# Kernel tuning notes

Measured on AMD Instinct MI355X. Metric: run time of the kernel, lower is better.

The kernel has to match this reference:

```python
import jax, jax.numpy as jnp
import numpy as np
import math

B, S, D = 8, 2048, 512
WINDOW = 30

def setup_inputs() -> dict:
    key = jax.random.key(0)
    ks = jax.random.split(key, 9)
    s = 1.0 / math.sqrt(D)
    return {
        "hidden_states": jax.random.normal(ks[0], (B, S, D), jnp.float32),
        "Wq": jax.random.normal(ks[1], (D, D), jnp.float32) * s,
        "bq": jax.random.normal(ks[2], (D,), jnp.float32) * s,
        "Wk": jax.random.normal(ks[3], (D, D), jnp.float32) * s,
        "bk": jax.random.normal(ks[4], (D,), jnp.float32) * s,
        "Wv": jax.random.normal(ks[5], (D, D), jnp.float32) * s,
        "bv": jax.random.normal(ks[6], (D,), jnp.float32) * s,
        "Wg": jax.random.normal(ks[7], (D, 1), jnp.float32) * s,
        "bg": jax.random.normal(ks[8], (1,), jnp.float32) * s,
    }

def reference(hidden_states, Wq, bq, Wk, bk, Wv, bv, Wg, bg):
    seq_len = hidden_states.shape[1]
    scale = math.sqrt(hidden_states.shape[-1])
    Q = hidden_states @ Wq + bq
    K = hidden_states @ Wk + bk
    V = hidden_states @ Wv + bv
    # [B, S, S] dense scores, single head
    scores = jnp.einsum('bsd,btd->bst', Q, K) / scale
    global_out = jnp.einsum('bst,btd->bsd', jax.nn.softmax(scores, axis=-1), V)
    pos = jnp.arange(seq_len)
    window_mask = jnp.abs(pos[:, None] - pos[None, :]) <= WINDOW  # [S, S]
    local_scores = scores + jnp.where(window_mask, 0.0, -1e9)
    local_out = jnp.einsum('bst,btd->bsd', jax.nn.softmax(local_scores, axis=-1), V)
    gate = jax.nn.sigmoid(hidden_states @ Wg + bg)  # [B, S, 1]
    return (1.0 - gate) * global_out + gate * local_out
```

## Files before the change

### kernel.cpp

```cpp
#include <hip/hip_runtime.h>
#include <math.h>

#define B_N   8
#define S_LEN 2048
#define D_DIM 512
#define M_TOT (B_N * S_LEN)
#define WIN   30

typedef short bf16x8 __attribute__((ext_vector_type(8)));
typedef float f32x4  __attribute__((ext_vector_type(4)));
typedef unsigned short u16;
typedef unsigned int   u32;

__device__ __forceinline__ u16 f2bf(float f) {
    union { float f; u32 u; } v; v.f = f;
    u32 r = v.u + 0x7fffu + ((v.u >> 16) & 1u);
    return (u16)(r >> 16);
}
__device__ __forceinline__ float bf2f(u16 u) {
    union { u32 u; float f; } v; v.u = ((u32)u) << 16; return v.f;
}

__device__ __forceinline__ void gl2lds(const u16* g, u16* l) {
    __builtin_amdgcn_global_load_lds((const __attribute__((address_space(1))) void*)g,
                                     (__attribute__((address_space(3))) void*)l,
                                     16, 0, 0);
}

__device__ __forceinline__ int xcd_logical() {
    const int n = gridDim.x;
    const int hb = blockIdx.x;
    return (hb & 7) * (n >> 3) + (hb >> 3);
}

#define VM_WAIT(N) asm volatile("s_waitcnt vmcnt(" #N ")" ::: "memory")
#define BAR() do { __builtin_amdgcn_s_barrier(); asm volatile("" ::: "memory"); } while (0)

__global__ __launch_bounds__(256)
void convert_gate(const float* __restrict__ X, const float* __restrict__ Wg,
                  const float* __restrict__ bg, u16* __restrict__ Xb, float* __restrict__ gate) {
    int wv = threadIdx.x >> 6, lane = threadIdx.x & 63;
    int row = blockIdx.x * 4 + wv;
    const float4* x4 = (const float4*)(X + (size_t)row * D_DIM);
    const float4* w4 = (const float4*)Wg;
    float acc = 0.f;
    ushort4 o0, o1;
    {
        float4 a = x4[lane * 2], w = w4[lane * 2];
        acc += a.x * w.x + a.y * w.y + a.z * w.z + a.w * w.w;
        o0.x = f2bf(a.x); o0.y = f2bf(a.y); o0.z = f2bf(a.z); o0.w = f2bf(a.w);
        float4 b = x4[lane * 2 + 1], v = w4[lane * 2 + 1];
        acc += b.x * v.x + b.y * v.y + b.z * v.z + b.w * v.w;
        o1.x = f2bf(b.x); o1.y = f2bf(b.y); o1.z = f2bf(b.z); o1.w = f2bf(b.w);
    }
    ushort4* xb4 = (ushort4*)(Xb + (size_t)row * D_DIM);
    xb4[lane * 2] = o0;
    xb4[lane * 2 + 1] = o1;
#pragma unroll
    for (int o = 32; o; o >>= 1) acc += __shfl_xor(acc, o);
    if (lane == 0) gate[row] = 1.f / (1.f + __expf(-(acc + bg[0])));
}

__global__ __launch_bounds__(256) void transpose_w3(const float* __restrict__ Wq, const float* __restrict__ Wk,
                                                    const float* __restrict__ Wv, u16* __restrict__ Wt3) {
    const float* W = blockIdx.z == 0 ? Wq : (blockIdx.z == 1 ? Wk : Wv);
    u16* Wt = Wt3 + (size_t)blockIdx.z * D_DIM * D_DIM;
    __shared__ float t[32][33];
    int k0 = blockIdx.x * 32, n0 = blockIdx.y * 32;
    int tx = threadIdx.x & 31, ty = threadIdx.x >> 5;
#pragma unroll
    for (int r = ty; r < 32; r += 8) t[r][tx] = W[(size_t)(k0 + r) * D_DIM + n0 + tx];
    __syncthreads();
#pragma unroll
    for (int r = ty; r < 32; r += 8) Wt[(size_t)(n0 + r) * D_DIM + k0 + tx] = f2bf(t[tx][r]);
}

__global__ __launch_bounds__(256) void pack_bias(const float* __restrict__ bq, const float* __restrict__ bk,
                                                 const float* __restrict__ bv, float* __restrict__ b3) {
    int i = blockIdx.x * 256 + threadIdx.x;
    b3[i] = bq[i]; b3[512 + i] = bk[i]; b3[1024 + i] = bv[i];
}

template<int EPI>
__global__ __launch_bounds__(512, 2)
void gemm256(const u16* __restrict__ A, const u16* __restrict__ Bt,
             int lda, int ldb, int K, int nx, int ny,
             const float* __restrict__ aux, void* __restrict__ Cv, int ldc, float scale,
             long long zA, long long zB, long long zC, long long zAux) {
    const int logical = xcd_logical();
    const int x = logical % nx;
    const int t2 = logical / nx;
    const int y = t2 % ny;
    const int z = t2 / ny;

    A   += zA * z;
    Bt  += zB * z;
    if (aux) aux += zAux * z;

    constexpr int BUF = 16384;
    __shared__ u16 smem[3 * BUF];
    const int tid  = threadIdx.x;
    const int lane = tid & 63;
    const int wave = tid >> 6;
    const int wr = wave >> 2, wc = wave & 3;
    const int m0 = y * 256, n0 = x * 256;

    f32x4 acc[8][4];
#pragma unroll
    for (int i = 0; i < 8; i++)
#pragma unroll
        for (int j = 0; j < 4; j++) acc[i][j] = (f32x4){0.f, 0.f, 0.f, 0.f};

    auto stage_h = [&](int b, int k0, int h) {
        int c2 = ((h & 1) << 9) + tid;
        int r  = c2 >> 2;
        int s  = (((c2 & 3) ^ ((c2 >> 3) & 3)) << 3);
        const u16* src = (h < 2) ? A  + (size_t)(m0 + r) * lda + (k0 + s)
                                 : Bt + (size_t)(n0 + r) * ldb + (k0 + s);
        gl2lds(src, smem + b * BUF + h * 4096 + wave * 512);
    };

    const int nt = K >> 5;
#pragma unroll
    for (int h = 0; h < 4; h++) stage_h(0, 0, h);
#pragma unroll
    for (int h = 0; h < 4; h++) stage_h(1, 32, h);

    const int ks = lane >> 4;
    for (int t = 0; t < nt; ++t) {
        const int cur = t % 3;
        const int nxt = (t + 2) % 3;
        const bool pf = (t + 2 < nt);
        const int kn = (t + 2) << 5;
        const u16* bA = smem + cur * BUF;
        const u16* bB = bA + 8192;

        bf16x8 af03[4], af47[4], b01[2], b23[2];

        if (t == nt - 1) { VM_WAIT(0); } else { VM_WAIT(4); }
        BAR();
        if (pf) stage_h(nxt, kn, 0);
#pragma unroll
        for (int n = 0; n < 2; n++) {
            int r = wc * 64 + n * 16 + (lane & 15);
            b01[n] = *(const bf16x8*)&bB[r * 32 + (ks ^ ((r >> 1) & 3)) * 8];
        }
#pragma unroll
        for (int m = 0; m < 4; m++) {
            int r = wr * 128 + m * 16 + (lane & 15);
            af03[m] = *(const bf16x8*)&bA[r * 32 + (ks ^ ((r >> 1) & 3)) * 8];
        }
        __builtin_amdgcn_s_setprio(1);
#pragma unroll
        for (int m = 0; m < 4; m++)
#pragma unroll
            for (int n = 0; n < 2; n++)
                acc[m][n] = __builtin_amdgcn_mfma_f32_16x16x32_bf16(af03[m], b01[n], acc[m][n], 0, 0, 0);
        __builtin_amdgcn_s_setprio(0);

        BAR();
        if (pf) stage_h(nxt, kn, 1);
#pragma unroll
        for (int n = 0; n < 2; n++) {
            int r = wc * 64 + (n + 2) * 16 + (lane & 15);
            b23[n] = *(const bf16x8*)&bB[r * 32 + (ks ^ ((r >> 1) & 3)) * 8];
        }
        __builtin_amdgcn_s_setprio(1);
#pragma unroll
        for (int m = 0; m < 4; m++)
#pragma unroll
            for (int n = 0; n < 2; n++)
                acc[m][n + 2] = __builtin_amdgcn_mfma_f32_16x16x32_bf16(af03[m], b23[n], acc[m][n + 2], 0, 0, 0);
        __builtin_amdgcn_s_setprio(0);

        BAR();
        if (pf) stage_h(nxt, kn, 2);
#pragma unroll
        for (int m = 0; m < 4; m++) {
            int r = wr * 128 + (m + 4) * 16 + (lane & 15);
            af47[m] = *(const bf16x8*)&bA[r * 32 + (ks ^ ((r >> 1) & 3)) * 8];
        }
        __builtin_amdgcn_s_setprio(1);
#pragma unroll
        for (int m = 0; m < 4; m++)
#pragma unroll
            for (int n = 0; n < 2; n++)
                acc[m + 4][n] = __builtin_amdgcn_mfma_f32_16x16x32_bf16(af47[m], b01[n], acc[m + 4][n], 0, 0, 0);
        __builtin_amdgcn_s_setprio(0);

        BAR();
        if (pf) stage_h(nxt, kn, 3);
        __builtin_amdgcn_s_setprio(1);
#pragma unroll
        for (int m = 0; m < 4; m++)
#pragma unroll
            for (int n = 0; n < 2; n++)
                acc[m + 4][n + 2] = __builtin_amdgcn_mfma_f32_16x16x32_bf16(af47[m], b23[n], acc[m + 4][n + 2], 0, 0, 0);
        __builtin_amdgcn_s_setprio(0);
    }

    u16* Cb = (u16*)Cv + zC * z;
#pragma unroll
    for (int m = 0; m < 8; m++) {
        int rbase = m0 + wr * 128 + m * 16 + ((lane >> 4) << 2);
#pragma unroll
        for (int n = 0; n < 4; n++) {
            int col = n0 + wc * 64 + n * 16 + (lane & 15);
#pragma unroll
            for (int rg = 0; rg < 4; rg++) {
                int row = rbase + rg;
                float v = acc[m][n][rg];
                if (EPI == 0) {
                    Cb[(size_t)row * ldc + col] = f2bf(v + aux[col]);
                } else {
                    Cb[(size_t)row * ldc + col] = f2bf(v * scale);
                }
            }
        }
    }
}

template<int EPI>
__global__ __launch_bounds__(256, 6)
void gemm_bt(const u16* __restrict__ A, const u16* __restrict__ Bt,
             int lda, int ldb, int K, int nx, int ny,
             const float* __restrict__ aux, void* __restrict__ Cv, int ldc, float scale,
             long long zA, long long zB, long long zC, long long zAux) {
    const int logical = xcd_logical();
    const int x = logical % nx;
    const int t2 = logical / nx;
    const int y = t2 % ny;
    const int z = t2 / ny;

    A   += zA * z;
    Bt  += zB * z;
    if (aux) aux += zAux * z;

    __shared__ u16 smem[3 * 8192];
    const int tid  = threadIdx.x;
    const int lane = tid & 63;
    const int wave = tid >> 6;
    const int wr = wave >> 1, wc = wave & 1;
    const int m0 = y * 128, n0 = x * 128;

    f32x4 acc[4][4];
#pragma unroll
    for (int i = 0; i < 4; i++)
#pragma unroll
        for (int j = 0; j < 4; j++) acc[i][j] = (f32x4){0.f, 0.f, 0.f, 0.f};

    const int c0 = tid, c1 = tid + 256;
    const int r0c = c0 >> 2, k0c = (((c0 & 3) ^ ((c0 >> 3) & 3)) << 3);
    const int r1c = c1 >> 2, k1c = (((c1 & 3) ^ ((c1 >> 3) & 3)) << 3);

    auto stage = [&](int b, int k0) {
        u16* dA = smem + b * 8192 + wave * 512;
        u16* dB = smem + b * 8192 + 4096 + wave * 512;
        gl2lds(A + (size_t)(m0 + r0c) * lda + (k0 + k0c), dA);
        gl2lds(A + (size_t)(m0 + r1c) * lda + (k0 + k1c), dA + 2048);
        gl2lds(Bt + (size_t)(n0 + r0c) * ldb + (k0 + k0c), dB);
        gl2lds(Bt + (size_t)(n0 + r1c) * ldb + (k0 + k1c), dB + 2048);
    };
    auto compute = [&](int b) {
        const u16* bA = smem + b * 8192;
        const u16* bB = smem + b * 8192 + 4096;
        const int ks = lane >> 4;
        bf16x8 af[4], bfr[4];
#pragma unroll
        for (int m = 0; m < 4; m++) {
            int r = wr * 64 + m * 16 + (lane & 15);
            af[m] = *(const bf16x8*)&bA[r * 32 + (ks ^ ((r >> 1) & 3)) * 8];
        }
#pragma unroll
        for (int n = 0; n < 4; n++) {
            int r = wc * 64 + n * 16 + (lane & 15);
            bfr[n] = *(const bf16x8*)&bB[r * 32 + (ks ^ ((r >> 1) & 3)) * 8];
        }
#pragma unroll
        for (int m = 0; m < 4; m++)
#pragma unroll
            for (int n = 0; n < 4; n++)
                acc[m][n] = __builtin_amdgcn_mfma_f32_16x16x32_bf16(af[m], bfr[n], acc[m][n], 0, 0, 0);
    };

    const int nt = K >> 5;
    stage(0, 0); stage(1, 32);

    int t = 0;
    for (; t < nt - 1; ++t) {
        VM_WAIT(4);
        BAR();
        if (t + 2 < nt) stage((t + 2) % 3, (t + 2) << 5);
        compute(t % 3);
    }
    VM_WAIT(0);
    BAR();
    compute((nt - 1) % 3);

    u16*   Cb = (EPI == 1) ? ((u16*)Cv + zC * z) : nullptr;
    float* Cf = (EPI == 2) ? ((float*)Cv + zC * z) : nullptr;

#pragma unroll
    for (int m = 0; m < 4; m++) {
        int rbase = m0 + wr * 64 + m * 16 + ((lane >> 4) << 2);
#pragma unroll
        for (int n = 0; n < 4; n++) {
            int col = n0 + wc * 64 + n * 16 + (lane & 15);
#pragma unroll
            for (int rg = 0; rg < 4; rg++) {
                int row = rbase + rg;
                float v = acc[m][n][rg];
                if (EPI == 1) {
                    Cb[(size_t)row * ldc + col] = f2bf(v + aux[row]);
                } else {
                    Cf[(size_t)row * ldc + col] = v * scale;
                }
            }
        }
    }
}

__global__ __launch_bounds__(256)
void softmax_fuse(u16* __restrict__ sc, const float* __restrict__ gate) {
    const int logical = xcd_logical();
    const int i = logical & (S_LEN - 1);
    const int z = logical >> 11;
    const int tid = threadIdx.x;
    const int wv = tid >> 6, lane = tid & 63;
    sc   += (size_t)z * S_LEN * S_LEN;
    gate += (size_t)z * S_LEN;

    __shared__ float r0[4], r1[4], mll[2];

    u16* scrow = sc + (size_t)i * S_LEN;
    uint4 raw = ((const uint4*)scrow)[tid];

    int jlo = i - WIN; if (jlo < 0) jlo = 0;
    int jhi = i + WIN; if (jhi > S_LEN - 1) jhi = S_LEN - 1;
    int cnt = jhi - jlo + 1;
    float bvv = (tid < cnt) ? bf2f(scrow[jlo + tid]) : -3.0e38f;
    float g = gate[i];

    float sv[8];
    sv[0] = bf2f((u16)(raw.x & 0xffff)); sv[1] = bf2f((u16)(raw.x >> 16));
    sv[2] = bf2f((u16)(raw.y & 0xffff)); sv[3] = bf2f((u16)(raw.y >> 16));
    sv[4] = bf2f((u16)(raw.z & 0xffff)); sv[5] = bf2f((u16)(raw.z >> 16));
    sv[6] = bf2f((u16)(raw.w & 0xffff)); sv[7] = bf2f((u16)(raw.w >> 16));

    float mx = fmaxf(fmaxf(fmaxf(sv[0], sv[1]), fmaxf(sv[2], sv[3])),
                     fmaxf(fmaxf(sv[4], sv[5]), fmaxf(sv[6], sv[7])));
#pragma unroll
    for (int o = 32; o; o >>= 1) mx = fmaxf(mx, __shfl_xor(mx, o));
    if (lane == 0) r0[wv] = mx;
    __syncthreads();
    float mg = fmaxf(fmaxf(r0[0], r0[1]), fmaxf(r0[2], r0[3]));

    float ev[8];
#pragma unroll
    for (int k = 0; k < 8; k++) ev[k] = __expf(sv[k] - mg);
    float se = ev[0] + ev[1] + ev[2] + ev[3] + ev[4] + ev[5] + ev[6] + ev[7];
#pragma unroll
    for (int o = 32; o; o >>= 1) se += __shfl_xor(se, o);
    if (lane == 0) r1[wv] = se;

    if (wv == 0) {
        float ml = bvv;
#pragma unroll
        for (int o = 32; o; o >>= 1) ml = fmaxf(ml, __shfl_xor(ml, o));
        float e = (lane < cnt) ? __expf(bvv - ml) : 0.f;
        float s2 = e;
#pragma unroll
        for (int o = 32; o; o >>= 1) s2 += __shfl_xor(s2, o);
        if (lane == 0) { mll[0] = ml; mll[1] = 1.f / s2; }
    }
    __syncthreads();
    float invl = (1.f - g) / (r1[0] + r1[1] + r1[2] + r1[3]);
    float ml  = mll[0];
    float ill = g * mll[1];

    const int c0 = tid * 8;
    u32 pk_[4];
#pragma unroll
    for (int h = 0; h < 4; h++) {
        float rA = ev[2 * h] * invl;
        float rB = ev[2 * h + 1] * invl;
        int colA = c0 + 2 * h;
        if ((u32)(colA - i + WIN) <= 2u * WIN)     rA += __expf(sv[2 * h] - ml) * ill;
        if ((u32)(colA + 1 - i + WIN) <= 2u * WIN) rB += __expf(sv[2 * h + 1] - ml) * ill;
        pk_[h] = (u32)f2bf(rA) | ((u32)f2bf(rB) << 16);
    }
    uint4 pw = {pk_[0], pk_[1], pk_[2], pk_[3]};
    ((uint4*)scrow)[tid] = pw;
}

extern "C" void kernel_launch(void* const* d_in, const int* in_sizes, int n_in,
                              void* d_out, int out_size, void* d_ws, size_t ws_size,
                              hipStream_t stream) {
    const float* X  = (const float*)d_in[0];
    const float* Wq = (const float*)d_in[1];
    const float* bq = (const float*)d_in[2];
    const float* Wk = (const float*)d_in[3];
    const float* bk = (const float*)d_in[4];
    const float* Wv = (const float*)d_in[5];
    const float* bv = (const float*)d_in[6];
    const float* Wg = (const float*)d_in[7];
    const float* bg = (const float*)d_in[8];
    float* out = (float*)d_out;

    char* p = (char*)d_ws;
    u16* Xb    = (u16*)p;  p += (size_t)M_TOT * D_DIM * 2;
    u16* Wt3   = (u16*)p;  p += (size_t)3 * D_DIM * D_DIM * 2;
    u16* QKV   = (u16*)p;  p += (size_t)2 * M_TOT * D_DIM * 2;
    u16* Vt    = (u16*)p;  p += (size_t)M_TOT * D_DIM * 2;
    float* gate  = (float*)p; p += (size_t)M_TOT * 4;
    float* bias3 = (float*)p; p += (size_t)3 * D_DIM * 4;
    u16* scores = (u16*)p;
    size_t base_used = (size_t)(p - (char*)d_ws);
    size_t per_batch = (size_t)S_LEN * S_LEN * 2;
    int nbuf = (int)((ws_size - base_used) / per_batch);
    if (nbuf > B_N) nbuf = B_N;
    if (nbuf < 1) nbuf = 1;

    u16* Qb = QKV;
    u16* Kb = QKV + (size_t)M_TOT * D_DIM;

    convert_gate<<<dim3(M_TOT / 4), 256, 0, stream>>>(X, Wg, bg, Xb, gate);
    transpose_w3<<<dim3(16, 16, 3), 256, 0, stream>>>(Wq, Wk, Wv, Wt3);
    pack_bias<<<dim3(2), 256, 0, stream>>>(bq, bk, bv, bias3);

    gemm256<0><<<dim3(2 * 64 * 2), 512, 0, stream>>>(
        Xb, Wt3, 512, 512, 512, 2, 64, bias3, QKV, 512, 1.f,
        0LL, (long long)D_DIM * D_DIM, (long long)M_TOT * D_DIM, (long long)D_DIM);

    gemm_bt<1><<<dim3(128 * 4), 256, 0, stream>>>(
        Wt3 + (size_t)2 * D_DIM * D_DIM, Xb, 512, 512, 512, 128, 4, bv, Vt, M_TOT, 1.f,
        0LL, 0LL, 0LL, 0LL);

    const float sc = 1.0f / sqrtf((float)D_DIM);
    for (int g0 = 0; g0 < B_N; g0 += nbuf) {
        int gcnt = B_N - g0 < nbuf ? B_N - g0 : nbuf;
        gemm256<3><<<dim3(8 * 8 * gcnt), 512, 0, stream>>>(
            Qb + (size_t)g0 * S_LEN * D_DIM, Kb + (size_t)g0 * S_LEN * D_DIM,
            512, 512, 512, 8, 8, nullptr, scores, S_LEN, sc,
            (long long)S_LEN * D_DIM, (long long)S_LEN * D_DIM,
            (long long)S_LEN * S_LEN, 0LL);
        softmax_fuse<<<dim3(S_LEN * gcnt), 256, 0, stream>>>(
            scores, gate + (size_t)g0 * S_LEN);
        gemm_bt<2><<<dim3(4 * 16 * gcnt), 256, 0, stream>>>(
            scores, Vt + (size_t)g0 * S_LEN,
            S_LEN, M_TOT, S_LEN, 4, 16, nullptr,
            out + (size_t)g0 * S_LEN * D_DIM, 512, 1.f,
            (long long)S_LEN * S_LEN, (long long)S_LEN,
            (long long)S_LEN * D_DIM, 0LL);
    }
}
```

Baseline: 175.5 us.

## Deepen gemm256 K-step to 64 with double-buffered quarter-tile prefetch schedule

Restructures the 256x256 GEMM main loop to process 64-wide K tiles with two LDS buffers of 64 KB each (128 KB total) instead of three 32-wide buffers. Loads are split into A/B halves that are prefetched at different sub-phases so each half-buffer is refilled as soon as its fragments are read into registers. Occupancy drops to one block per CU because of the larger shared-memory footprint and register arrays. The aim is fewer barriers per unit of K and better overlap of global-to-LDS loads with MFMA work, at the cost of latency hiding across blocks.

```diff
diff --git a/kernel.cpp b/kernel.cpp
--- a/kernel.cpp
+++ b/kernel.cpp
@@ -82,7 +82,7 @@
 }
 
 template<int EPI>
-__global__ __launch_bounds__(512, 2)
+__global__ __launch_bounds__(512, 1)
 void gemm256(const u16* __restrict__ A, const u16* __restrict__ Bt,
              int lda, int ldb, int K, int nx, int ny,
              const float* __restrict__ aux, void* __restrict__ Cv, int ldc, float scale,
@@ -97,13 +97,13 @@
     Bt  += zB * z;
     if (aux) aux += zAux * z;
 
-    constexpr int BUF = 16384;
-    __shared__ u16 smem[3 * BUF];
+    __shared__ u16 smem[65536];
     const int tid  = threadIdx.x;
     const int lane = tid & 63;
     const int wave = tid >> 6;
     const int wr = wave >> 2, wc = wave & 3;
     const int m0 = y * 256, n0 = x * 256;
+    const int ks = lane >> 4, l15 = lane & 15;
 
     f32x4 acc[8][4];
 #pragma unroll
@@ -111,92 +111,128 @@
 #pragma unroll
         for (int j = 0; j < 4; j++) acc[i][j] = (f32x4){0.f, 0.f, 0.f, 0.f};
 
-    auto stage_h = [&](int b, int k0, int h) {
-        int c2 = ((h & 1) << 9) + tid;
-        int r  = c2 >> 2;
-        int s  = (((c2 & 3) ^ ((c2 >> 3) & 3)) << 3);
-        const u16* src = (h < 2) ? A  + (size_t)(m0 + r) * lda + (k0 + s)
-                                 : Bt + (size_t)(n0 + r) * ldb + (k0 + s);
-        gl2lds(src, smem + b * BUF + h * 4096 + wave * 512);
+    auto stA = [&](int buf, int k0, int alpha) {
+#pragma unroll
+        for (int j = 0; j < 2; j++) {
+            int c = j * 512 + tid;
+            int rr = (c >> 2) & 127;
+            int row = (rr & 63) + ((rr & 64) << 1) + (alpha << 6);
+            int gk = k0 + j * 32 + (((c & 3) ^ ((row >> 1) & 3)) << 3);
+            int rr0 = wave << 4;
+            int row0 = (rr0 & 63) + ((rr0 & 64) << 1) + (alpha << 6);
+            gl2lds(A + (size_t)(m0 + row) * lda + gk,
+                   smem + buf * 32768 + j * 8192 + row0 * 32);
+        }
     };
-
-    const int nt = K >> 5;
-#pragma unroll
-    for (int h = 0; h < 4; h++) stage_h(0, 0, h);
-#pragma unroll
-    for (int h = 0; h < 4; h++) stage_h(1, 32, h);
-
-    const int ks = lane >> 4;
+    auto stB = [&](int buf, int k0, int beta) {
+#pragma unroll
+        for (int j = 0; j < 2; j++) {
+            int c = j * 512 + tid;
+            int rr = (c >> 2) & 127;
+            int row = (rr & 31) + ((rr >> 5) << 6) + (beta << 5);
+            int gk = k0 + j * 32 + (((c & 3) ^ ((row >> 1) & 3)) << 3);
+            int rr0 = wave << 4;
+            int row0 = (rr0 & 31) + ((rr0 >> 5) << 6) + (beta << 5);
+            gl2lds(Bt + (size_t)(n0 + row) * ldb + gk,
+                   smem + buf * 32768 + 16384 + j * 8192 + row0 * 32);
+        }
+    };
+
+    const int nt = K >> 6;
+    stA(0, 0, 0); stB(0, 0, 0); stB(0, 0, 1); stA(0, 0, 1);
+    stA(1, 64, 0); stB(1, 64, 0);
+    VM_WAIT(8);
+    BAR();
+
     for (int t = 0; t < nt; ++t) {
-        const int cur = t % 3;
-        const int nxt = (t + 2) % 3;
-        const bool pf = (t + 2 < nt);
-        const int kn = (t + 2) << 5;
-        const u16* bA = smem + cur * BUF;
-        const u16* bB = bA + 8192;
-
-        bf16x8 af03[4], af47[4], b01[2], b23[2];
-
-        if (t == nt - 1) { VM_WAIT(0); } else { VM_WAIT(4); }
-        BAR();
-        if (pf) stage_h(nxt, kn, 0);
-#pragma unroll
-        for (int n = 0; n < 2; n++) {
-            int r = wc * 64 + n * 16 + (lane & 15);
-            b01[n] = *(const bf16x8*)&bB[r * 32 + (ks ^ ((r >> 1) & 3)) * 8];
-        }
-#pragma unroll
-        for (int m = 0; m < 4; m++) {
-            int r = wr * 128 + m * 16 + (lane & 15);
-            af03[m] = *(const bf16x8*)&bA[r * 32 + (ks ^ ((r >> 1) & 3)) * 8];
-        }
+        const int cur = t & 1;
+        const u16* bA = smem + cur * 32768;
+        const u16* bB = bA + 16384;
+        const int kn1 = (t + 1) << 6, kn2 = (t + 2) << 6;
+        bf16x8 A03[4][2], A47[4][2], B01[2][2], B23[2][2];
+
+        if (t == nt - 1) { VM_WAIT(2); } else { VM_WAIT(6); }
+#pragma unroll
+        for (int m = 0; m < 4; m++)
+#pragma unroll
+            for (int kk = 0; kk < 2; kk++) {
+                int r = wr * 128 + m * 16 + l15;
+                A03[m][kk] = *(const bf16x8*)&bA[kk * 8192 + r * 32 + ((ks ^ ((r >> 1) & 3)) << 3)];
+            }
+#pragma unroll
+        for (int n = 0; n < 2; n++)
+#pragma unroll
+            for (int kk = 0; kk < 2; kk++) {
+                int r = wc * 64 + n * 16 + l15;
+                B01[n][kk] = *(const bf16x8*)&bB[kk * 8192 + r * 32 + ((ks ^ ((r >> 1) & 3)) << 3)];
+            }
+        if (t + 1 < nt) stB(cur ^ 1, kn1, 1);
+        BAR();
         __builtin_amdgcn_s_setprio(1);
 #pragma unroll
         for (int m = 0; m < 4; m++)
 #pragma unroll
-            for (int n = 0; n < 2; n++)
-                acc[m][n] = __builtin_amdgcn_mfma_f32_16x16x32_bf16(af03[m], b01[n], acc[m][n], 0, 0, 0);
+            for (int n = 0; n < 2; n++) {
+                acc[m][n] = __builtin_amdgcn_mfma_f32_16x16x32_bf16(A03[m][0], B01[n][0], acc[m][n], 0, 0, 0);
+                acc[m][n] = __builtin_amdgcn_mfma_f32_16x16x32_bf16(A03[m][1], B01[n][1], acc[m][n], 0, 0, 0);
+            }
         __builtin_amdgcn_s_setprio(0);
-
-        BAR();
-        if (pf) stage_h(nxt, kn, 1);
-#pragma unroll
-        for (int n = 0; n < 2; n++) {
-            int r = wc * 64 + (n + 2) * 16 + (lane & 15);
-            b23[n] = *(const bf16x8*)&bB[r * 32 + (ks ^ ((r >> 1) & 3)) * 8];
-        }
+        BAR();
+
+        if (t == nt - 1) { VM_WAIT(0); } else { VM_WAIT(6); }
+#pragma unroll
+        for (int n = 0; n < 2; n++)
+#pragma unroll
+            for (int kk = 0; kk < 2; kk++) {
+                int r = wc * 64 + (n + 2) * 16 + l15;
+                B23[n][kk] = *(const bf16x8*)&bB[kk * 8192 + r * 32 + ((ks ^ ((r >> 1) & 3)) << 3)];
+            }
+        if (t + 1 < nt) stA(cur ^ 1, kn1, 1);
+        BAR();
         __builtin_amdgcn_s_setprio(1);
 #pragma unroll
         for (int m = 0; m < 4; m++)
 #pragma unroll
-            for (int n = 0; n < 2; n++)
-                acc[m][n + 2] = __builtin_amdgcn_mfma_f32_16x16x32_bf16(af03[m], b23[n], acc[m][n + 2], 0, 0, 0);
+            for (int n = 0; n < 2; n++) {
+                acc[m][n + 2] = __builtin_amdgcn_mfma_f32_16x16x32_bf16(A03[m][0], B23[n][0], acc[m][n + 2], 0, 0, 0);
+                acc[m][n + 2] = __builtin_amdgcn_mfma_f32_16x16x32_bf16(A03[m][1], B23[n][1], acc[m][n + 2], 0, 0, 0);
+            }
         __builtin_amdgcn_s_setprio(0);
-
-        BAR();
-        if (pf) stage_h(nxt, kn, 2);
-#pragma unroll
-        for (int m = 0; m < 4; m++) {
-            int r = wr * 128 + (m + 4) * 16 + (lane & 15);
-            af47[m] = *(const bf16x8*)&bA[r * 32 + (ks ^ ((r >> 1) & 3)) * 8];
-        }
+        BAR();
+
+#pragma unroll
+        for (int m = 0; m < 4; m++)
+#pragma unroll
+            for (int kk = 0; kk < 2; kk++) {
+                int r = wr * 128 + (m + 4) * 16 + l15;
+                A47[m][kk] = *(const bf16x8*)&bA[kk * 8192 + r * 32 + ((ks ^ ((r >> 1) & 3)) << 3)];
+            }
+        if (t + 2 < nt) stA(cur, kn2, 0);
+        BAR();
         __builtin_amdgcn_s_setprio(1);
 #pragma unroll
         for (int m = 0; m < 4; m++)
 #pragma unroll
-            for (int n = 0; n < 2; n++)
-                acc[m + 4][n] = __builtin_amdgcn_mfma_f32_16x16x32_bf16(af47[m], b01[n], acc[m + 4][n], 0, 0, 0);
+            for (int n = 0; n < 2; n++) {
+                acc[m + 4][n + 2] = __builtin_amdgcn_mfma_f32_16x16x32_bf16(A47[m][0], B23[n][0], acc[m + 4][n + 2], 0, 0, 0);
+                acc[m + 4][n + 2] = __builtin_amdgcn_mfma_f32_16x16x32_bf16(A47[m][1], B23[n][1], acc[m + 4][n + 2], 0, 0, 0);
+            }
         __builtin_amdgcn_s_setprio(0);
-
-        BAR();
-        if (pf) stage_h(nxt, kn, 3);
+        BAR();
+
+        if (t == nt - 2) { VM_WAIT(4); } else if (t < nt - 2) { VM_WAIT(6); }
+        if (t + 2 < nt) stB(cur, kn2, 0);
+        BAR();
         __builtin_amdgcn_s_setprio(1);
 #pragma unroll
         for (int m = 0; m < 4; m++)
 #pragma unroll
-            for (int n = 0; n < 2; n++)
-                acc[m + 4][n + 2] = __builtin_amdgcn_mfma_f32_16x16x32_bf16(af47[m], b23[n], acc[m + 4][n + 2], 0, 0, 0);
+            for (int n = 0; n < 2; n++) {
+                acc[m + 4][n] = __builtin_amdgcn_mfma_f32_16x16x32_bf16(A47[m][0], B01[n][0], acc[m + 4][n], 0, 0, 0);
+                acc[m + 4][n] = __builtin_amdgcn_mfma_f32_16x16x32_bf16(A47[m][1], B01[n][1], acc[m + 4][n], 0, 0, 0);
+            }
         __builtin_amdgcn_s_setprio(0);
+        BAR();
     }
 
     u16* Cb = (u16*)Cv + zC * z;
@@ -205,7 +241,7 @@
         int rbase = m0 + wr * 128 + m * 16 + ((lane >> 4) << 2);
 #pragma unroll
         for (int n = 0; n < 4; n++) {
-            int col = n0 + wc * 64 + n * 16 + (lane & 15);
+            int col = n0 + wc * 64 + n * 16 + l15;
 #pragma unroll
             for (int rg = 0; rg < 4; rg++) {
                 int row = rbase + rg;
```

Measured after the change: 169.5 us. -3.4%, faster.
